# Performance work log

Hardware: AMD Instinct MI355X
Metric: run time of the kernel (lower is better)

## Reference

```python
import jax, jax.numpy as jnp
import numpy as np

H = 2048      # hidden_size
I = 8192      # dense intermediate_size
MI = 1024     # moe_intermediate_size
E = 8         # num_local_experts
K = 2         # num_experts_per_tok
B, S = 2, 1024
EPS = 1e-6
ROOT = H ** (-0.5)


def _rms(x, w=None, eps=EPS):
    # fp32 RMSNorm matching _Gemma4CPURMSNorm; w=None -> no-scale variant
    ms = jnp.mean(x * x, axis=-1, keepdims=True) + eps
    y = x * jax.lax.rsqrt(ms)
    return y * w if w is not None else y


def _gelu_tanh(x):
    # gelu_pytorch_tanh == tanh-approximate gelu
    return jax.nn.gelu(x, approximate=True)


def setup_inputs() -> dict:
    key = jax.random.key(0)
    ks = jax.random.split(key, 10)
    s = 0.02
    return {
        "hidden_states": jax.random.normal(ks[0], (B, S, H), jnp.float32),
        # RMSNorm scales (init ones, as in nn.Parameter(torch.ones(dim)))
        "rn_pre1": jnp.ones((H,), jnp.float32),
        "rn_pre2": jnp.ones((H,), jnp.float32),
        "rn_post1": jnp.ones((H,), jnp.float32),
        "rn_post2": jnp.ones((H,), jnp.float32),
        "rn_post": jnp.ones((H,), jnp.float32),
        # dense GLU MLP weights, stored (in, out)
        "w_gate": jax.random.normal(ks[1], (H, I), jnp.float32) * s,
        "w_up":   jax.random.normal(ks[2], (H, I), jnp.float32) * s,
        "w_down": jax.random.normal(ks[3], (I, H), jnp.float32) * s,
        # router
        "router_w": jax.random.normal(ks[4], (H, E), jnp.float32) * s,
        "router_scale": jnp.ones((H,), jnp.float32),
        "per_expert_scale": jnp.ones((E,), jnp.float32),
        # per-expert GLU weights, stacked over experts
        "we_gate": jax.random.normal(ks[5], (E, H, MI), jnp.float32) * s,
        "we_up":   jax.random.normal(ks[6], (E, H, MI), jnp.float32) * s,
        "we_down": jax.random.normal(ks[7], (E, MI, H), jnp.float32) * s,
    }


def reference(hidden_states, rn_pre1, rn_pre2, rn_post1, rn_post2, rn_post,
              w_gate, w_up, w_down, router_w, router_scale, per_expert_scale,
              we_gate, we_up, we_down):
    b, s, h = hidden_states.shape
    T = b * s

    # --- dense branch ---
    dense_in = _rms(hidden_states, rn_pre1)                      # (B,S,H)
    dense_out = (_gelu_tanh(dense_in @ w_gate) * (dense_in @ w_up)) @ w_down
    dense_out = _rms(dense_out, rn_post1)                        # (B,S,H)

    # --- router (takes the raw residual, applies its own no-scale RMSNorm) ---
    x = hidden_states.reshape(T, h)
    xr = _rms(x) * router_scale * ROOT                           # (T,H)
    router_logits = xr @ router_w                                # (T,E)
    probs = jax.nn.softmax(router_logits, axis=-1)
    top_w, top_i = jax.lax.top_k(probs, K)                       # (T,K)
    top_w = top_w / jnp.sum(top_w, axis=-1, keepdims=True)
    top_w = top_w * per_expert_scale[top_i]
    aff = jnp.zeros((T, E), x.dtype).at[jnp.arange(T)[:, None], top_i].set(top_w)

    # --- MoE experts (compute all experts, combine with sparse affinities) ---
    moe_in = _rms(hidden_states, rn_pre2).reshape(T, h)          # (T,H)
    g = jnp.einsum('th,ehm->tem', moe_in, we_gate)               # (T,E,MI)
    u = jnp.einsum('th,ehm->tem', moe_in, we_up)
    eo = jnp.einsum('tem,emh->teh', _gelu_tanh(g) * u, we_down)  # (T,E,H)
    moe_out = jnp.einsum('te,teh->th', aff, eo).reshape(b, s, h)
    moe_out = _rms(moe_out, rn_post2)

    return _rms(dense_out + moe_out, rn_post)
```

## Files before the change

### kernel.cpp

```cpp
#include <hip/hip_runtime.h>
#include <stdint.h>

#define TOK 2048
#define HD  2048
#define ID  8192
#define ID2 16384
#define MID 1024
#define NE  8
#define KSPLIT 4

typedef __attribute__((ext_vector_type(8))) short s16x8;
typedef __attribute__((ext_vector_type(4))) short s16x4;
typedef __attribute__((ext_vector_type(4))) float f32x4;

constexpr float EPSF  = 1e-6f;
constexpr float ROOTF = 0.02209708691207961f;

#define MFMA(a, b, c) __builtin_amdgcn_mfma_f32_16x16x32_bf16(a, b, c, 0, 0, 0)
#define BAR() __builtin_amdgcn_s_barrier()
#define SCHED0() __builtin_amdgcn_sched_barrier(0)
#define VMCNT(n) asm volatile("s_waitcnt vmcnt(" #n ")" ::: "memory")

__device__ __forceinline__ void gload16(const void* g, void* l) {
  __builtin_amdgcn_global_load_lds(
      (const __attribute__((address_space(1))) void*)g,
      (__attribute__((address_space(3))) void*)l, 16, 0, 0);
}

__device__ __forceinline__ short f2bf(float f) {
  union { float f; uint32_t u; } v; v.f = f;
  uint32_t r = v.u + 0x7fffu + ((v.u >> 16) & 1u);
  return (short)(r >> 16);
}

__device__ __forceinline__ float bf2f(short s) {
  union { uint32_t u; float f; } v; v.u = ((uint32_t)(uint16_t)s) << 16;
  return v.f;
}

__device__ __forceinline__ float gelu_tanh(float x) {
  float x3 = x * x * x;
  float u = 0.7978845608028654f * (x + 0.044715f * x3);
  return 0.5f * x * (1.0f + tanhf(u));
}

__global__ __launch_bounds__(256) void k_rms_router(
    const float* __restrict__ x, const float* __restrict__ rnp1,
    const float* __restrict__ rnp2, const float* __restrict__ rsc,
    const float* __restrict__ rw, const float* __restrict__ pes,
    short* __restrict__ rms1, short* __restrict__ rms2,
    int* __restrict__ cnt, int* __restrict__ tokl,
    float* __restrict__ wgtl, int* __restrict__ slotl) {
  const int t = blockIdx.x, tid = threadIdx.x;
  const size_t base = (size_t)t * HD;
  f32x4 v[2];
  float ss = 0.f;
#pragma unroll
  for (int i = 0; i < 2; ++i) {
    v[i] = *(const f32x4*)(x + base + tid * 4 + i * 1024);
#pragma unroll
    for (int j = 0; j < 4; ++j) ss += v[i][j] * v[i][j];
  }
  __shared__ float sr[4];
  __shared__ float sl[32];
#pragma unroll
  for (int off = 32; off; off >>= 1) ss += __shfl_down(ss, off, 64);
  if ((tid & 63) == 0) sr[tid >> 6] = ss;
  __syncthreads();
  const float inv = rsqrtf((sr[0] + sr[1] + sr[2] + sr[3]) * (1.0f / HD) + EPSF);
  float p[8] = {0, 0, 0, 0, 0, 0, 0, 0};
#pragma unroll
  for (int i = 0; i < 2; ++i) {
    const int h = tid * 4 + i * 1024;
    f32x4 w1 = *(const f32x4*)(rnp1 + h);
    f32x4 w2 = *(const f32x4*)(rnp2 + h);
    f32x4 sc = *(const f32x4*)(rsc + h);
    s16x4 o1, o2;
#pragma unroll
    for (int j = 0; j < 4; ++j) {
      float xn = v[i][j] * inv;
      o1[j] = f2bf(xn * w1[j]);
      o2[j] = f2bf(xn * w2[j]);
      float xq = xn * sc[j] * ROOTF;
      const float* rr = rw + (size_t)(h + j) * NE;
      f32x4 ra = *(const f32x4*)rr;
      f32x4 rb = *(const f32x4*)(rr + 4);
      p[0] += xq * ra[0]; p[1] += xq * ra[1]; p[2] += xq * ra[2]; p[3] += xq * ra[3];
      p[4] += xq * rb[0]; p[5] += xq * rb[1]; p[6] += xq * rb[2]; p[7] += xq * rb[3];
    }
    *(s16x4*)(rms1 + base + h) = o1;
    *(s16x4*)(rms2 + base + h) = o2;
  }
#pragma unroll
  for (int e = 0; e < 8; ++e)
#pragma unroll
    for (int off = 32; off; off >>= 1) p[e] += __shfl_down(p[e], off, 64);
  if ((tid & 63) == 0) {
#pragma unroll
    for (int e = 0; e < 8; ++e) sl[(tid >> 6) * 8 + e] = p[e];
  }
  __syncthreads();
  if (tid == 0) {
    float l[8];
#pragma unroll
    for (int e = 0; e < 8; ++e) l[e] = sl[e] + sl[8 + e] + sl[16 + e] + sl[24 + e];
    int i1 = 0;
#pragma unroll
    for (int e = 1; e < 8; ++e) if (l[e] > l[i1]) i1 = e;
    int i2 = (i1 == 0) ? 1 : 0;
#pragma unroll
    for (int e = 0; e < 8; ++e) if (e != i1 && l[e] > l[i2]) i2 = e;
    float p2 = expf(l[i2] - l[i1]);
    float s = 1.0f + p2;
    float w1 = (1.0f / s) * pes[i1];
    float w2 = (p2 / s) * pes[i2];
    int q1 = atomicAdd(&cnt[i1], 1);
    tokl[i1 * TOK + q1] = t; wgtl[i1 * TOK + q1] = w1; slotl[i1 * TOK + q1] = 0;
    int q2 = atomicAdd(&cnt[i2], 1);
    tokl[i2 * TOK + q2] = t; wgtl[i2 * TOK + q2] = w2; slotl[i2 * TOK + q2] = 1;
  }
}

__global__ __launch_bounds__(256) void k_transpose(
    const float* __restrict__ in, short* __restrict__ out, int R, int C) {
  __shared__ float tile[64 * 65];
  const int tid = threadIdx.x;
  const int c0 = blockIdx.x * 64, r0 = blockIdx.y * 64;
  const size_t bo = (size_t)blockIdx.z * R * C;
#pragma unroll
  for (int i = 0; i < 4; ++i) {
    int idx = tid + 256 * i;
    int r = idx >> 4, c4 = idx & 15;
    f32x4 f = *(const f32x4*)(in + bo + (size_t)(r0 + r) * C + c0 + c4 * 4);
#pragma unroll
    for (int j = 0; j < 4; ++j) tile[(c4 * 4 + j) * 65 + r] = f[j];
  }
  __syncthreads();
#pragma unroll
  for (int i = 0; i < 2; ++i) {
    int ch = tid + 256 * i;
    int c = ch >> 3, rs = ch & 7;
    s16x8 o;
#pragma unroll
    for (int q = 0; q < 8; ++q) o[q] = f2bf(tile[c * 65 + rs * 8 + q]);
    *(s16x8*)(out + bo + (size_t)(c0 + c) * R + r0 + rs * 8) = o;
  }
}

__global__ __launch_bounds__(512, 2) void k_gemm256(
    const short* __restrict__ Wt,
    const short* __restrict__ X,
    short* __restrict__ C) {
  __shared__ char lds[2][65536];
  const int tid = threadIdx.x;
  const int lane = tid & 63, wave = tid >> 6;
  const int wr = wave >> 2, wc = wave & 3;
  const int ln15 = lane & 15, l16 = lane >> 4;
  const int lin = blockIdx.y * 64 + blockIdx.x;
  const int lin2 = (lin & 7) * 64 + (lin >> 3);
  const int m0 = (lin2 & 63) * 256, t0 = (lin2 >> 6) * 256;
  const int swz = (ln15 & 7) << 4;
  const int srow = tid >> 3;
  const int sslot = ((tid & 7) ^ ((tid >> 3) & 7)) << 4;
  const char* Wb = (const char*)Wt;
  const char* Xb = (const char*)X;
  auto STAGE = [&](int kt, int s) {
#pragma unroll
    for (int c = 0; c < 4; ++c) {
      gload16(Wb + (size_t)(m0 + c * 64 + srow) * 4096 + kt * 128 + sslot,
              &lds[s][c * 8192] + wave * 1024);
      gload16(Xb + (size_t)(t0 + c * 64 + srow) * 4096 + kt * 128 + sslot,
              &lds[s][32768 + c * 8192] + wave * 1024);
    }
  };
  f32x4 acc[8][4];
#pragma unroll
  for (int m = 0; m < 8; ++m)
#pragma unroll
    for (int n = 0; n < 4; ++n) acc[m][n] = (f32x4)0.f;
  const int NT = HD / 64;
  STAGE(0, 0);
  STAGE(1, 1);
  VMCNT(8);
  SCHED0();
  BAR();
#pragma unroll 2
  for (int kt = 0; kt < NT; ++kt) {
    const int s = kt & 1;
    const char* sA = &lds[s][0];
    const char* sB = &lds[s][32768];
#pragma unroll
    for (int ks = 0; ks < 2; ++ks) {
      const int ka = (ks * 64 + l16 * 16) ^ swz;
      s16x8 b[4];
#pragma unroll
      for (int n = 0; n < 4; ++n)
        b[n] = *(const s16x8*)(sB + (wc * 64 + n * 16 + ln15) * 128 + ka);
#pragma unroll
      for (int mh = 0; mh < 2; ++mh) {
        s16x8 a[4];
#pragma unroll
        for (int f = 0; f < 4; ++f)
          a[f] = *(const s16x8*)(sA + (wr * 128 + mh * 64 + f * 16 + ln15) * 128 + ka);
        __builtin_amdgcn_s_setprio(1);
#pragma unroll
        for (int f = 0; f < 4; ++f)
#pragma unroll
          for (int n = 0; n < 4; ++n)
            acc[mh * 4 + f][n] = MFMA(a[f], b[n], acc[mh * 4 + f][n]);
        __builtin_amdgcn_s_setprio(0);
      }
    }
    BAR();
    if (kt + 2 < NT) {
      STAGE(kt + 2, s);
      VMCNT(8);
    } else if (kt + 1 < NT) {
      VMCNT(0);
    }
    SCHED0();
    BAR();
  }
#pragma unroll
  for (int mi = 0; mi < 8; ++mi)
#pragma unroll
    for (int n = 0; n < 4; ++n) {
      const int t = t0 + wc * 64 + n * 16 + ln15;
      const int i = m0 + wr * 128 + mi * 16 + l16 * 4;
      s16x4 o;
#pragma unroll
      for (int r = 0; r < 4; ++r) o[r] = f2bf(acc[mi][n][r]);
      *(s16x4*)(C + (size_t)t * ID2 + i) = o;
    }
}

__global__ __launch_bounds__(512, 2) void k_dd256(
    const short* __restrict__ Wd,
    const short* __restrict__ X,
    short* __restrict__ dparts) {
  __shared__ char lds[2][65536];
  const int tid = threadIdx.x;
  const int lane = tid & 63, wave = tid >> 6;
  const int wr = wave >> 2, wc = wave & 3;
  const int ln15 = lane & 15, l16 = lane >> 4;
  const int m0 = blockIdx.x * 256, t0 = blockIdx.y * 256;
  const size_t kB = (size_t)blockIdx.z * 4096;
  const int swz = (ln15 & 7) << 4;
  const int srow = tid >> 3;
  const int sslot = ((tid & 7) ^ ((tid >> 3) & 7)) << 4;
  const char* Wb = (const char*)Wd;
  const char* Xb = (const char*)X;
  auto STAGE = [&](int kt, int s) {
#pragma unroll
    for (int c = 0; c < 4; ++c) {
      gload16(Wb + (size_t)(m0 + c * 64 + srow) * 16384 + kB + kt * 128 + sslot,
              &lds[s][c * 8192] + wave * 1024);
      gload16(Xb + (size_t)(t0 + c * 64 + srow) * 16384 + kB + kt * 128 + sslot,
              &lds[s][32768 + c * 8192] + wave * 1024);
    }
  };
  f32x4 acc[8][4];
#pragma unroll
  for (int m = 0; m < 8; ++m)
#pragma unroll
    for (int n = 0; n < 4; ++n) acc[m][n] = (f32x4)0.f;
  const int NT = (ID / KSPLIT) / 64;
  STAGE(0, 0);
  STAGE(1, 1);
  VMCNT(8);
  SCHED0();
  BAR();
#pragma unroll 2
  for (int kt = 0; kt < NT; ++kt) {
    const int s = kt & 1;
    const char* sA = &lds[s][0];
    const char* sB = &lds[s][32768];
#pragma unroll
    for (int ks = 0; ks < 2; ++ks) {
      const int ka = (ks * 64 + l16 * 16) ^ swz;
      s16x8 b[4];
#pragma unroll
      for (int n = 0; n < 4; ++n)
        b[n] = *(const s16x8*)(sB + (wc * 64 + n * 16 + ln15) * 128 + ka);
#pragma unroll
      for (int mh = 0; mh < 2; ++mh) {
        s16x8 a[4];
#pragma unroll
        for (int f = 0; f < 4; ++f)
          a[f] = *(const s16x8*)(sA + (wr * 128 + mh * 64 + f * 16 + ln15) * 128 + ka);
        __builtin_amdgcn_s_setprio(1);
#pragma unroll
        for (int f = 0; f < 4; ++f)
#pragma unroll
          for (int n = 0; n < 4; ++n)
            acc[mh * 4 + f][n] = MFMA(a[f], b[n], acc[mh * 4 + f][n]);
        __builtin_amdgcn_s_setprio(0);
      }
    }
    BAR();
    if (kt + 2 < NT) {
      STAGE(kt + 2, s);
      VMCNT(8);
    } else if (kt + 1 < NT) {
      VMCNT(0);
    }
    SCHED0();
    BAR();
  }
  short* dst = dparts + (size_t)blockIdx.z * TOK * HD;
#pragma unroll
  for (int mi = 0; mi < 8; ++mi)
#pragma unroll
    for (int n = 0; n < 4; ++n) {
      const int t = t0 + wc * 64 + n * 16 + ln15;
      const int h = m0 + wr * 128 + mi * 16 + l16 * 4;
      s16x4 o;
#pragma unroll
      for (int r = 0; r < 4; ++r) o[r] = f2bf(acc[mi][n][r]);
      *(s16x4*)(dst + (size_t)t * HD + h) = o;
    }
}

__global__ __launch_bounds__(256) void k_gelumul(
    const short* __restrict__ cbuf, short* __restrict__ o) {
  const int flat = blockIdx.x * 256 + threadIdx.x;
  const int t = flat >> 10;
  const int i8 = (flat & 1023) * 8;
  const short* g = cbuf + (size_t)t * ID2 + i8;
  s16x8 gv = *(const s16x8*)g;
  s16x8 uv = *(const s16x8*)(g + ID);
  s16x8 ov;
#pragma unroll
  for (int j = 0; j < 8; ++j)
    ov[j] = f2bf(gelu_tanh(bf2f(gv[j])) * bf2f(uv[j]));
  *(s16x8*)(o + (size_t)t * ID + i8) = ov;
}

__global__ __launch_bounds__(256) void k_exp_gateup(
    const short* __restrict__ wegT, const short* __restrict__ weuT,
    const short* __restrict__ rms2,
    const int* __restrict__ cnt, const int* __restrict__ tokl,
    short* __restrict__ acte) {
  const int e = blockIdx.z;
  const int cn = cnt[e];
  const int t0 = blockIdx.y * 128;
  if (t0 >= cn) return;
  const int n0 = blockIdx.x * 64;
  __shared__ short sW[128 * 32];
  __shared__ short sX[128 * 32];
  const int tid = threadIdx.x;
  const int lane = tid & 63, wave = tid >> 6;
  const int ln15 = lane & 15, k8 = (lane >> 4) * 8;
  const int nsub = (wave & 1) * 32, tsub = (wave >> 1) * 64;
  const int srow = tid >> 2, skc = (tid & 3) * 8;
  const int* tl = tokl + e * TOK;
  int r0 = t0 + srow, r1 = t0 + 64 + srow;
  int tk0 = tl[r0 < cn ? r0 : cn - 1];
  int tk1 = tl[r1 < cn ? r1 : cn - 1];
  const short* gW0 = wegT + (size_t)e * MID * HD + (size_t)(n0 + srow) * HD + skc;
  const short* gW1 = weuT + (size_t)e * MID * HD + (size_t)(n0 + srow) * HD + skc;
  const short* gX0 = rms2 + (size_t)tk0 * HD + skc;
  const short* gX1 = rms2 + (size_t)tk1 * HD + skc;
  char* lW = (char*)sW + wave * 1024;
  char* lX = (char*)sX + wave * 1024;
  f32x4 accg[2][4], accu[2][4];
#pragma unroll
  for (int m = 0; m < 2; ++m)
#pragma unroll
    for (int n = 0; n < 4; ++n) { accg[m][n] = (f32x4)0.f; accu[m][n] = (f32x4)0.f; }
  for (int kt = 0; kt < HD / 32; ++kt) {
    const int ko = kt * 32;
    __syncthreads();
    gload16(gW0 + ko, lW);
    gload16(gW1 + ko, lW + 4096);
    gload16(gX0 + ko, lX);
    gload16(gX1 + ko, lX + 4096);
    __syncthreads();
    s16x8 ag[2], au[2], bx[4];
#pragma unroll
    for (int m = 0; m < 2; ++m) {
      ag[m] = *(const s16x8*)(sW + (nsub + m * 16 + ln15) * 32 + k8);
      au[m] = *(const s16x8*)(sW + (64 + nsub + m * 16 + ln15) * 32 + k8);
    }
#pragma unroll
    for (int n = 0; n < 4; ++n)
      bx[n] = *(const s16x8*)(sX + (tsub + n * 16 + ln15) * 32 + k8);
#pragma unroll
    for (int m = 0; m < 2; ++m)
#pragma unroll
      for (int n = 0; n < 4; ++n) {
        accg[m][n] = MFMA(ag[m], bx[n], accg[m][n]);
        accu[m][n] = MFMA(au[m], bx[n], accu[m][n]);
      }
  }
#pragma unroll
  for (int m = 0; m < 2; ++m)
#pragma unroll
    for (int n = 0; n < 4; ++n) {
      const int r = t0 + tsub + n * 16 + ln15;
      if (r < cn) {
        const int ib = n0 + nsub + m * 16 + (lane >> 4) * 4;
        s16x4 o;
#pragma unroll
        for (int q = 0; q < 4; ++q)
          o[q] = f2bf(gelu_tanh(accg[m][n][q]) * accu[m][n][q]);
        *(s16x4*)(acte + (size_t)e * TOK * MID + (size_t)r * MID + ib) = o;
      }
    }
}

__global__ __launch_bounds__(256) void k_exp_down(
    const short* __restrict__ wedT,
    const short* __restrict__ acte,
    const int* __restrict__ cnt, const int* __restrict__ tokl,
    const float* __restrict__ wgtl, const int* __restrict__ slotl,
    float* __restrict__ moep) {
  const int e = blockIdx.z;
  const int cn = cnt[e];
  const int t0 = blockIdx.y * 128;
  if (t0 >= cn) return;
  const int n0 = blockIdx.x * 128;
  __shared__ short sW[128 * 32];
  __shared__ short sX[128 * 32];
  const int tid = threadIdx.x;
  const int lane = tid & 63, wave = tid >> 6;
  const int wr = wave >> 1, wc = wave & 1;
  const int ln15 = lane & 15, k8 = (lane >> 4) * 8;
  const int srow = tid >> 2, skc = (tid & 3) * 8;
  const short* wb = wedT + (size_t)e * HD * MID;
  const short* gW0 = wb + (size_t)(n0 + srow) * MID + skc;
  const short* gW1 = wb + (size_t)(n0 + 64 + srow) * MID + skc;
  const short* ab = acte + (size_t)e * TOK * MID;
  const short* gX0 = ab + (size_t)(t0 + srow) * MID + skc;
  const short* gX1 = ab + (size_t)(t0 + 64 + srow) * MID + skc;
  char* lW = (char*)sW + wave * 1024;
  char* lX = (char*)sX + wave * 1024;
  f32x4 acc[4][4];
#pragma unroll
  for (int m = 0; m < 4; ++m)
#pragma unroll
    for (int n = 0; n < 4; ++n) acc[m][n] = (f32x4)0.f;
  for (int kt = 0; kt < MID / 32; ++kt) {
    const int ko = kt * 32;
    __syncthreads();
    gload16(gW0 + ko, lW);
    gload16(gW1 + ko, lW + 4096);
    gload16(gX0 + ko, lX);
    gload16(gX1 + ko, lX + 4096);
    __syncthreads();
    s16x8 a[4], b[4];
#pragma unroll
    for (int m = 0; m < 4; ++m)
      a[m] = *(const s16x8*)(sW + (wr * 64 + m * 16 + ln15) * 32 + k8);
#pragma unroll
    for (int n = 0; n < 4; ++n)
      b[n] = *(const s16x8*)(sX + (wc * 64 + n * 16 + ln15) * 32 + k8);
#pragma unroll
    for (int m = 0; m < 4; ++m)
#pragma unroll
      for (int n = 0; n < 4; ++n) acc[m][n] = MFMA(a[m], b[n], acc[m][n]);
  }
#pragma unroll
  for (int n = 0; n < 4; ++n) {
    const int r = t0 + wc * 64 + n * 16 + ln15;
    if (r < cn) {
      const int tk = tokl[e * TOK + r];
      const float wf = wgtl[e * TOK + r];
      const int sl = slotl[e * TOK + r];
      float* dst = moep + (size_t)sl * TOK * HD + (size_t)tk * HD;
#pragma unroll
      for (int m = 0; m < 4; ++m) {
        const int h = n0 + wr * 64 + m * 16 + (lane >> 4) * 4;
        f32x4 v = acc[m][n] * wf;
        *(f32x4*)(dst + h) = v;
      }
    }
  }
}

__global__ __launch_bounds__(256) void k_final(
    const short* __restrict__ dparts,
    const float* __restrict__ moep,
    const float* __restrict__ rno1, const float* __restrict__ rno2,
    const float* __restrict__ rnof, float* __restrict__ out) {
  const int t = blockIdx.x, tid = threadIdx.x;
  const size_t base = (size_t)t * HD;
  f32x4 dv[2], mv[2];
  float ssd = 0.f, ssm = 0.f;
#pragma unroll
  for (int i = 0; i < 2; ++i) {
    const int h = tid * 4 + i * 1024;
    dv[i] = (f32x4)0.f;
#pragma unroll
    for (int z = 0; z < KSPLIT; ++z) {
      s16x4 d4 = *(const s16x4*)(dparts + (size_t)z * TOK * HD + base + h);
#pragma unroll
      for (int j = 0; j < 4; ++j) dv[i][j] += bf2f(d4[j]);
    }
    f32x4 a = *(const f32x4*)(moep + base + h);
    f32x4 b = *(const f32x4*)(moep + (size_t)TOK * HD + base + h);
    mv[i] = a + b;
#pragma unroll
    for (int j = 0; j < 4; ++j) { ssd += dv[i][j] * dv[i][j]; ssm += mv[i][j] * mv[i][j]; }
  }
  __shared__ float sr[8];
#pragma unroll
  for (int off = 32; off; off >>= 1) {
    ssd += __shfl_down(ssd, off, 64);
    ssm += __shfl_down(ssm, off, 64);
  }
  if ((tid & 63) == 0) { sr[tid >> 6] = ssd; sr[4 + (tid >> 6)] = ssm; }
  __syncthreads();
  const float invd = rsqrtf((sr[0] + sr[1] + sr[2] + sr[3]) * (1.0f / HD) + EPSF);
  const float invm = rsqrtf((sr[4] + sr[5] + sr[6] + sr[7]) * (1.0f / HD) + EPSF);
  f32x4 y[2];
  float ssy = 0.f;
#pragma unroll
  for (int i = 0; i < 2; ++i) {
    const int h = tid * 4 + i * 1024;
    f32x4 w1 = *(const f32x4*)(rno1 + h);
    f32x4 w2 = *(const f32x4*)(rno2 + h);
#pragma unroll
    for (int j = 0; j < 4; ++j) {
      y[i][j] = dv[i][j] * invd * w1[j] + mv[i][j] * invm * w2[j];
      ssy += y[i][j] * y[i][j];
    }
  }
  __syncthreads();
#pragma unroll
  for (int off = 32; off; off >>= 1) ssy += __shfl_down(ssy, off, 64);
  if ((tid & 63) == 0) sr[tid >> 6] = ssy;
  __syncthreads();
  const float invy = rsqrtf((sr[0] + sr[1] + sr[2] + sr[3]) * (1.0f / HD) + EPSF);
#pragma unroll
  for (int i = 0; i < 2; ++i) {
    const int h = tid * 4 + i * 1024;
    f32x4 w = *(const f32x4*)(rnof + h);
    f32x4 o;
#pragma unroll
    for (int j = 0; j < 4; ++j) o[j] = y[i][j] * invy * w[j];
    *(f32x4*)(out + base + h) = o;
  }
}

extern "C" void kernel_launch(void* const* d_in, const int* in_sizes, int n_in,
                              void* d_out, int out_size, void* d_ws, size_t ws_size,
                              hipStream_t stream) {
  (void)in_sizes; (void)n_in; (void)out_size;
  const float* x    = (const float*)d_in[0];
  const float* rnp1 = (const float*)d_in[1];
  const float* rnp2 = (const float*)d_in[2];
  const float* rno1 = (const float*)d_in[3];
  const float* rno2 = (const float*)d_in[4];
  const float* rnof = (const float*)d_in[5];
  const float* wg   = (const float*)d_in[6];
  const float* wu   = (const float*)d_in[7];
  const float* wd   = (const float*)d_in[8];
  const float* rw   = (const float*)d_in[9];
  const float* rsc  = (const float*)d_in[10];
  const float* pes  = (const float*)d_in[11];
  const float* weg  = (const float*)d_in[12];
  const float* weu  = (const float*)d_in[13];
  const float* wed  = (const float*)d_in[14];
  float* out = (float*)d_out;

  char* ws = (char*)d_ws;
  size_t off = 0;
  auto alloc = [&](size_t bytes) -> void* {
    void* p = ws + off;
    off += (bytes + 255) & ~(size_t)255;
    return p;
  };
  const size_t IH  = (size_t)ID * HD;
  const size_t EMH = (size_t)NE * MID * HD;
  short* wgT   = (short*)alloc(IH * 2);
  short* wuT   = (short*)alloc(IH * 2);
  short* wdT   = (short*)alloc(IH * 2);
  short* wegT  = (short*)alloc(EMH * 2);
  short* weuT  = (short*)alloc(EMH * 2);
  short* wedT  = (short*)alloc(EMH * 2);
  short* rms1  = (short*)alloc((size_t)TOK * HD * 2);
  short* rms2  = (short*)alloc((size_t)TOK * HD * 2);
  short* actb  = (short*)alloc((size_t)TOK * ID * 2);
  short* acte  = (short*)alloc((size_t)NE * TOK * MID * 2);
  float* moep  = (float*)alloc((size_t)2 * TOK * HD * 4);
  int*   cnt   = (int*)alloc(NE * 4);
  int*   tokl  = (int*)alloc((size_t)NE * TOK * 4);
  float* wgtl  = (float*)alloc((size_t)NE * TOK * 4);
  int*   slotl = (int*)alloc((size_t)NE * TOK * 4);
  if (off > ws_size) return;
  short* dparts = (short*)wgT;
  short* cbuf = acte;

  hipMemsetAsync(cnt, 0, NE * 4, stream);
  k_rms_router<<<TOK, 256, 0, stream>>>(x, rnp1, rnp2, rsc, rw, pes,
                                        rms1, rms2, cnt, tokl, wgtl, slotl);
  k_transpose<<<dim3(ID / 64, HD / 64, 1), 256, 0, stream>>>(wg, wgT, HD, ID);
  k_transpose<<<dim3(ID / 64, HD / 64, 1), 256, 0, stream>>>(wu, wuT, HD, ID);
  k_transpose<<<dim3(HD / 64, ID / 64, 1), 256, 0, stream>>>(wd, wdT, ID, HD);
  k_transpose<<<dim3(MID / 64, HD / 64, NE), 256, 0, stream>>>(weg, wegT, HD, MID);
  k_transpose<<<dim3(MID / 64, HD / 64, NE), 256, 0, stream>>>(weu, weuT, HD, MID);
  k_transpose<<<dim3(HD / 64, MID / 64, NE), 256, 0, stream>>>(wed, wedT, MID, HD);
  k_gemm256<<<dim3(ID2 / 256, TOK / 256), 512, 0, stream>>>(wgT, rms1, cbuf);
  k_gelumul<<<(TOK * ID) / (256 * 8), 256, 0, stream>>>(cbuf, actb);
  k_dd256<<<dim3(HD / 256, TOK / 256, KSPLIT), 512, 0, stream>>>(wdT, actb, dparts);
  k_exp_gateup<<<dim3(MID / 64, TOK / 128, NE), 256, 0, stream>>>(wegT, weuT, rms2,
                                                                  cnt, tokl, acte);
  k_exp_down<<<dim3(HD / 128, TOK / 128, NE), 256, 0, stream>>>(wedT, acte, cnt, tokl,
                                                                wgtl, slotl, moep);
  k_final<<<TOK, 256, 0, stream>>>(dparts, moep, rno1, rno2, rnof, out);
}
```

Measured before the change: 554.6 us.

## Use 4-stage K=32 LDS pipeline with new swizzle in GEMM kernels

Both 256x256 bf16 GEMM kernels (gate/up and down projection) move from a 2-stage double buffer with K=64 per stage to a 4-stage ring with K=32 per stage, prefetching three tiles ahead. The LDS row pitch drops to 64 bytes with a new XOR swizzle, and all 8 A fragments are loaded before one MFMA burst per stage. The grouped block-index remap for L2 locality in the gate/up GEMM is dropped in favour of a plain grid mapping. The aim is to hide global-load latency better, at the cost of twice as many barriers per K and possible L2 locality loss.

```diff
diff --git a/kernel.cpp b/kernel.cpp
--- a/kernel.cpp
+++ b/kernel.cpp
@@ -151,26 +151,24 @@
     const short* __restrict__ Wt,
     const short* __restrict__ X,
     short* __restrict__ C) {
-  __shared__ char lds[2][65536];
+  __shared__ char lds[4][32768];
   const int tid = threadIdx.x;
   const int lane = tid & 63, wave = tid >> 6;
   const int wr = wave >> 2, wc = wave & 3;
   const int ln15 = lane & 15, l16 = lane >> 4;
-  const int lin = blockIdx.y * 64 + blockIdx.x;
-  const int lin2 = (lin & 7) * 64 + (lin >> 3);
-  const int m0 = (lin2 & 63) * 256, t0 = (lin2 >> 6) * 256;
-  const int swz = (ln15 & 7) << 4;
-  const int srow = tid >> 3;
-  const int sslot = ((tid & 7) ^ ((tid >> 3) & 7)) << 4;
+  const int m0 = blockIdx.x * 256, t0 = blockIdx.y * 256;
+  const int r0 = wave * 16 + (lane >> 2);
+  const int gks = (((lane & 3) ^ ((r0 >> 1) & 3)) << 4);
+  const int rsw = ((ln15 >> 1) & 3) << 4;
   const char* Wb = (const char*)Wt;
   const char* Xb = (const char*)X;
   auto STAGE = [&](int kt, int s) {
 #pragma unroll
-    for (int c = 0; c < 4; ++c) {
-      gload16(Wb + (size_t)(m0 + c * 64 + srow) * 4096 + kt * 128 + sslot,
+    for (int c = 0; c < 2; ++c) {
+      gload16(Wb + (size_t)(m0 + c * 128 + r0) * 4096 + kt * 64 + gks,
               &lds[s][c * 8192] + wave * 1024);
-      gload16(Xb + (size_t)(t0 + c * 64 + srow) * 4096 + kt * 128 + sslot,
-              &lds[s][32768 + c * 8192] + wave * 1024);
+      gload16(Xb + (size_t)(t0 + c * 128 + r0) * 4096 + kt * 64 + gks,
+              &lds[s][16384 + c * 8192] + wave * 1024);
     }
   };
   f32x4 acc[8][4];
@@ -178,46 +176,35 @@
   for (int m = 0; m < 8; ++m)
 #pragma unroll
     for (int n = 0; n < 4; ++n) acc[m][n] = (f32x4)0.f;
-  const int NT = HD / 64;
-  STAGE(0, 0);
-  STAGE(1, 1);
+  const int NT = HD / 32;
+  STAGE(0, 0); STAGE(1, 1); STAGE(2, 2);
   VMCNT(8);
   SCHED0();
   BAR();
-#pragma unroll 2
+#pragma unroll 4
   for (int kt = 0; kt < NT; ++kt) {
-    const int s = kt & 1;
+    const int s = kt & 3;
     const char* sA = &lds[s][0];
-    const char* sB = &lds[s][32768];
-#pragma unroll
-    for (int ks = 0; ks < 2; ++ks) {
-      const int ka = (ks * 64 + l16 * 16) ^ swz;
-      s16x8 b[4];
+    const char* sB = &lds[s][16384];
+    const int ka = (l16 << 4) ^ rsw;
+    s16x8 a[8], b[4];
+#pragma unroll
+    for (int m = 0; m < 8; ++m)
+      a[m] = *(const s16x8*)(sA + (wr * 128 + m * 16 + ln15) * 64 + ka);
+#pragma unroll
+    for (int n = 0; n < 4; ++n)
+      b[n] = *(const s16x8*)(sB + (wc * 64 + n * 16 + ln15) * 64 + ka);
+    __builtin_amdgcn_s_setprio(1);
+#pragma unroll
+    for (int m = 0; m < 8; ++m)
 #pragma unroll
       for (int n = 0; n < 4; ++n)
-        b[n] = *(const s16x8*)(sB + (wc * 64 + n * 16 + ln15) * 128 + ka);
-#pragma unroll
-      for (int mh = 0; mh < 2; ++mh) {
-        s16x8 a[4];
-#pragma unroll
-        for (int f = 0; f < 4; ++f)
-          a[f] = *(const s16x8*)(sA + (wr * 128 + mh * 64 + f * 16 + ln15) * 128 + ka);
-        __builtin_amdgcn_s_setprio(1);
-#pragma unroll
-        for (int f = 0; f < 4; ++f)
-#pragma unroll
-          for (int n = 0; n < 4; ++n)
-            acc[mh * 4 + f][n] = MFMA(a[f], b[n], acc[mh * 4 + f][n]);
-        __builtin_amdgcn_s_setprio(0);
-      }
-    }
+        acc[m][n] = MFMA(a[m], b[n], acc[m][n]);
+    __builtin_amdgcn_s_setprio(0);
     BAR();
-    if (kt + 2 < NT) {
-      STAGE(kt + 2, s);
-      VMCNT(8);
-    } else if (kt + 1 < NT) {
-      VMCNT(0);
-    }
+    if (kt + 3 < NT)       { STAGE(kt + 3, (kt + 3) & 3); VMCNT(8); }
+    else if (kt + 3 == NT) { VMCNT(4); }
+    else if (kt + 2 == NT) { VMCNT(0); }
     SCHED0();
     BAR();
   }
@@ -238,25 +225,25 @@
     const short* __restrict__ Wd,
     const short* __restrict__ X,
     short* __restrict__ dparts) {
-  __shared__ char lds[2][65536];
+  __shared__ char lds[4][32768];
   const int tid = threadIdx.x;
   const int lane = tid & 63, wave = tid >> 6;
   const int wr = wave >> 2, wc = wave & 3;
   const int ln15 = lane & 15, l16 = lane >> 4;
   const int m0 = blockIdx.x * 256, t0 = blockIdx.y * 256;
   const size_t kB = (size_t)blockIdx.z * 4096;
-  const int swz = (ln15 & 7) << 4;
-  const int srow = tid >> 3;
-  const int sslot = ((tid & 7) ^ ((tid >> 3) & 7)) << 4;
+  const int r0 = wave * 16 + (lane >> 2);
+  const int gks = (((lane & 3) ^ ((r0 >> 1) & 3)) << 4);
+  const int rsw = ((ln15 >> 1) & 3) << 4;
   const char* Wb = (const char*)Wd;
   const char* Xb = (const char*)X;
   auto STAGE = [&](int kt, int s) {
 #pragma unroll
-    for (int c = 0; c < 4; ++c) {
-      gload16(Wb + (size_t)(m0 + c * 64 + srow) * 16384 + kB + kt * 128 + sslot,
+    for (int c = 0; c < 2; ++c) {
+      gload16(Wb + (size_t)(m0 + c * 128 + r0) * 16384 + kB + kt * 64 + gks,
               &lds[s][c * 8192] + wave * 1024);
-      gload16(Xb + (size_t)(t0 + c * 64 + srow) * 16384 + kB + kt * 128 + sslot,
-              &lds[s][32768 + c * 8192] + wave * 1024);
+      gload16(Xb + (size_t)(t0 + c * 128 + r0) * 16384 + kB + kt * 64 + gks,
+              &lds[s][16384 + c * 8192] + wave * 1024);
     }
   };
   f32x4 acc[8][4];
@@ -264,46 +251,35 @@
   for (int m = 0; m < 8; ++m)
 #pragma unroll
     for (int n = 0; n < 4; ++n) acc[m][n] = (f32x4)0.f;
-  const int NT = (ID / KSPLIT) / 64;
-  STAGE(0, 0);
-  STAGE(1, 1);
+  const int NT = (ID / KSPLIT) / 32;
+  STAGE(0, 0); STAGE(1, 1); STAGE(2, 2);
   VMCNT(8);
   SCHED0();
   BAR();
-#pragma unroll 2
+#pragma unroll 4
   for (int kt = 0; kt < NT; ++kt) {
-    const int s = kt & 1;
+    const int s = kt & 3;
     const char* sA = &lds[s][0];
-    const char* sB = &lds[s][32768];
-#pragma unroll
-    for (int ks = 0; ks < 2; ++ks) {
-      const int ka = (ks * 64 + l16 * 16) ^ swz;
-      s16x8 b[4];
+    const char* sB = &lds[s][16384];
+    const int ka = (l16 << 4) ^ rsw;
+    s16x8 a[8], b[4];
+#pragma unroll
+    for (int m = 0; m < 8; ++m)
+      a[m] = *(const s16x8*)(sA + (wr * 128 + m * 16 + ln15) * 64 + ka);
+#pragma unroll
+    for (int n = 0; n < 4; ++n)
+      b[n] = *(const s16x8*)(sB + (wc * 64 + n * 16 + ln15) * 64 + ka);
+    __builtin_amdgcn_s_setprio(1);
+#pragma unroll
+    for (int m = 0; m < 8; ++m)
 #pragma unroll
       for (int n = 0; n < 4; ++n)
-        b[n] = *(const s16x8*)(sB + (wc * 64 + n * 16 + ln15) * 128 + ka);
-#pragma unroll
-      for (int mh = 0; mh < 2; ++mh) {
-        s16x8 a[4];
-#pragma unroll
-        for (int f = 0; f < 4; ++f)
-          a[f] = *(const s16x8*)(sA + (wr * 128 + mh * 64 + f * 16 + ln15) * 128 + ka);
-        __builtin_amdgcn_s_setprio(1);
-#pragma unroll
-        for (int f = 0; f < 4; ++f)
-#pragma unroll
-          for (int n = 0; n < 4; ++n)
-            acc[mh * 4 + f][n] = MFMA(a[f], b[n], acc[mh * 4 + f][n]);
-        __builtin_amdgcn_s_setprio(0);
-      }
-    }
+        acc[m][n] = MFMA(a[m], b[n], acc[m][n]);
+    __builtin_amdgcn_s_setprio(0);
     BAR();
-    if (kt + 2 < NT) {
-      STAGE(kt + 2, s);
-      VMCNT(8);
-    } else if (kt + 1 < NT) {
-      VMCNT(0);
-    }
+    if (kt + 3 < NT)       { STAGE(kt + 3, (kt + 3) & 3); VMCNT(8); }
+    else if (kt + 3 == NT) { VMCNT(4); }
+    else if (kt + 2 == NT) { VMCNT(0); }
     SCHED0();
     BAR();
   }
```

Result: no change. 551.6 us (-0.5%).
